# Kernel optimization log

Hardware: AMD Instinct MI355X
Metric: run time of the kernel (lower is better)

The kernel has to match this reference:

```python
import jax, jax.numpy as jnp
import numpy as np

H = 7      # n_hazards
B = 8      # batch
S = 2048   # seq_len
D = 768    # hidden_dim
K = 64     # bottleneck_dim
THR = 0.05 # influence_threshold


def setup_inputs() -> dict:
    key = jax.random.key(0)
    k0, k1, k2, k3 = jax.random.split(key, 4)
    x = jax.random.normal(k0, (H, B, S, D), jnp.float32)          # stacked hazard reprs
    M = jax.random.normal(k1, (H, H), jnp.float32) * 0.3           # interaction_matrix [src, tgt]
    W1 = jax.random.normal(k2, (H, H, D, K), jnp.float32) * (1.0 / np.sqrt(D).astype(np.float32))
    b1 = jnp.zeros((H, H, K), jnp.float32)
    W2 = jax.random.normal(k3, (H, H, K, D), jnp.float32) * (1.0 / np.sqrt(K).astype(np.float32))
    b2 = jnp.zeros((H, H, D), jnp.float32)
    return {"x": x, "M": M, "W1": W1, "b1": b1, "W2": W2, "b2": b2}


def reference(x, M, W1, b1, W2, b2):
    # Gate: influence used only if |M[s,t]| > threshold and s != t (torch skips the
    # projection entirely below threshold; masking to 0 yields identical values/grads).
    eye = jnp.eye(H, dtype=bool)
    gate = jnp.where((jnp.abs(M) > THR) & (~eye), M, jnp.zeros_like(M))  # [s, t]

    # Bottleneck MLP for all (source, target) pairs in one batched GEMM.
    # h: [s, t, b, n, k]
    h = jnp.einsum('sbnd,stdk->stbnk', x, W1) + b1[:, :, None, None, :]
    h = jax.nn.gelu(h, approximate=False)  # torch nn.GELU default is exact (erf)

    # Fold the scalar gate into the second GEMM so the [s,t,b,n,D] tensor is never
    # materialized; sum over sources lands directly at each target.
    add = jnp.einsum('st,stbnk,stkd->tbnd', gate, h, W2)
    add = add + jnp.einsum('st,std->td', gate, b2)[:, None, None, :]
    return x + add  # [H, B, S, D] stacked in hazard order
```

## Files before the change

### kernel.cpp

```cpp
#include <hip/hip_runtime.h>
#include <hip/hip_bf16.h>
#include <math.h>

#define NH   7
#define NROW 16384
#define DD   768
#define KK   64
#define THRG 0.05f

typedef float  f32x4   __attribute__((ext_vector_type(4)));
typedef __bf16 bf16x8  __attribute__((ext_vector_type(8)));
typedef short  short8v __attribute__((ext_vector_type(8)));
typedef short  short4v __attribute__((ext_vector_type(4)));

union V8 { short8v s; bf16x8 b; };

__device__ __forceinline__ unsigned short f2bf(float f) {
  unsigned u = __float_as_uint(f);
  u = (u + 0x7FFFu + ((u >> 16) & 1u)) >> 16;
  return (unsigned short)u;
}

__device__ __forceinline__ float gate_of(const float* __restrict__ M, int s, int t) {
  float m = M[s * NH + t];
  return (s != t && fabsf(m) > THRG) ? m : 0.0f;
}

__device__ __forceinline__ float gelu_t(float v) {
  float u = 0.7978845608028654f * (v + 0.044715f * v * v * v);
  return v / (1.0f + __expf(-2.0f * u));
}

__global__ void prep_w1(const float* __restrict__ W1, unsigned short* __restrict__ W1P) {
  int pr = blockIdx.x;
  const float* src = W1 + (size_t)pr * DD * KK;
  unsigned short* dst = W1P + (size_t)pr * 12 * 4096;
  for (int idx = threadIdx.x; idx < 12 * 64 * 64; idx += blockDim.x) {
    int kc = idx >> 12, rem = idx & 4095;
    int kcol = rem >> 6, dl = rem & 63;
    dst[idx] = f2bf(src[(size_t)(kc * 64 + dl) * KK + kcol]);
  }
}

__global__ void prep_w2(const float* __restrict__ M, const float* __restrict__ W2,
                        unsigned short* __restrict__ W2P) {
  int st = blockIdx.x;
  int s = st / NH, t = st % NH;
  float g = gate_of(M, s, t);
  const float* src = W2 + (size_t)st * KK * DD;
  unsigned short* dst = W2P + (size_t)((t * NH + s) * 6) * 8192;
  for (int idx = threadIdx.x; idx < 6 * 128 * 64; idx += blockDim.x) {
    int nb = idx >> 13, rem = idx & 8191;
    int dloc = rem >> 6, k = rem & 63;
    dst[idx] = f2bf(g * src[(size_t)k * DD + nb * 128 + dloc]);
  }
}

__global__ void prep_b2(const float* __restrict__ M, const float* __restrict__ b2,
                        float* __restrict__ b2sum) {
  int idx = blockIdx.x * blockDim.x + threadIdx.x;
  if (idx >= NH * DD) return;
  int t = idx / DD, d = idx % DD;
  float acc = 0.f;
  for (int s = 0; s < NH; ++s)
    acc += gate_of(M, s, t) * b2[(size_t)(s * NH + t) * DD + d];
  b2sum[idx] = acc;
}

__global__ __launch_bounds__(256, 3)
void chiA(const float* __restrict__ x, const float* __restrict__ M,
          const unsigned short* __restrict__ W1P, const float* __restrict__ b1,
          unsigned short* __restrict__ H) {
  __shared__ __align__(16) unsigned short xs[128 * 64];
  __shared__ __align__(16) unsigned short w1s[64 * 64];

  int bid = (int)blockIdx.x;
  int nid = (bid & 7) * 784 + (bid >> 3);
  int rb = nid / 49, pr = nid % 49;
  int s = pr / NH, t = pr % NH;
  if (gate_of(M, s, t) == 0.0f) return;
  int row0 = rb * 128;

  int tid = (int)threadIdx.x;
  int wid = tid >> 6, lane = tid & 63, l16 = lane & 15, l4 = lane >> 4;

  const f32x4 zero = {0.f, 0.f, 0.f, 0.f};
  f32x4 acc[4][2];
#pragma unroll
  for (int m = 0; m < 4; ++m)
#pragma unroll
    for (int n = 0; n < 2; ++n) acc[m][n] = zero;

  const float* xb = x + ((size_t)s * NROW + row0) * DD;
  const unsigned short* w1b = W1P + (size_t)pr * 12 * 4096;

  for (int kc = 0; kc < 12; ++kc) {
    __syncthreads();
#pragma unroll
    for (int r = 0; r < 4; ++r) {
      int L = r * 4096 + tid * 16;
      int row = L >> 7, colB = L & 127;
      const float* gp = xb + (size_t)row * DD + kc * 64 + (colB >> 1);
      f32x4 v0 = *(const f32x4*)gp;
      f32x4 v1 = *(const f32x4*)(gp + 4);
      short8v sv;
      sv[0] = (short)f2bf(v0[0]); sv[1] = (short)f2bf(v0[1]);
      sv[2] = (short)f2bf(v0[2]); sv[3] = (short)f2bf(v0[3]);
      sv[4] = (short)f2bf(v1[0]); sv[5] = (short)f2bf(v1[1]);
      sv[6] = (short)f2bf(v1[2]); sv[7] = (short)f2bf(v1[3]);
      *(short8v*)((char*)xs + (L ^ ((row & 7) << 4))) = sv;
    }
#pragma unroll
    for (int r = 0; r < 2; ++r) {
      int L = r * 4096 + tid * 16;
      int row = L >> 7;
      short8v v = *(const short8v*)((const char*)w1b + (size_t)kc * 8192 + L);
      *(short8v*)((char*)w1s + (L ^ ((row & 7) << 4))) = v;
    }
    __syncthreads();

    V8 af[4][2], bf2[2][2];
#pragma unroll
    for (int mm = 0; mm < 4; ++mm)
#pragma unroll
      for (int k2 = 0; k2 < 2; ++k2) {
        int rowl = mm * 16 + l16;
        int byte = (rowl * 128 + k2 * 64 + l4 * 16) ^ ((rowl & 7) << 4);
        af[mm][k2].s = *(const short8v*)((const char*)w1s + byte);
      }
#pragma unroll
    for (int nn = 0; nn < 2; ++nn)
#pragma unroll
      for (int k2 = 0; k2 < 2; ++k2) {
        int xr = wid * 32 + nn * 16 + l16;
        int byte = (xr * 128 + k2 * 64 + l4 * 16) ^ ((xr & 7) << 4);
        bf2[nn][k2].s = *(const short8v*)((const char*)xs + byte);
      }
#pragma unroll
    for (int k2 = 0; k2 < 2; ++k2)
#pragma unroll
      for (int mm = 0; mm < 4; ++mm)
#pragma unroll
        for (int nn = 0; nn < 2; ++nn)
          acc[mm][nn] = __builtin_amdgcn_mfma_f32_16x16x32_bf16(af[mm][k2].b, bf2[nn][k2].b, acc[mm][nn], 0, 0, 0);
  }

#pragma unroll
  for (int mm = 0; mm < 4; ++mm) {
    f32x4 bv = *(const f32x4*)(b1 + (size_t)pr * KK + mm * 16 + l4 * 4);
#pragma unroll
    for (int nn = 0; nn < 2; ++nn) {
      short4v o;
#pragma unroll
      for (int r = 0; r < 4; ++r) o[r] = (short)f2bf(gelu_t(acc[mm][nn][r] + bv[r]));
      int xrow = row0 + wid * 32 + nn * 16 + l16;
      unsigned short* hp = H + ((size_t)pr * NROW + xrow) * KK + mm * 16 + l4 * 4;
      *(short4v*)hp = o;
    }
  }
}

__global__ __launch_bounds__(256, 3)
void chiB(const unsigned short* __restrict__ H, const float* __restrict__ x,
          const float* __restrict__ M, const unsigned short* __restrict__ W2P,
          const float* __restrict__ b2sum, float* __restrict__ out) {
  __shared__ __align__(16) unsigned short hs[128 * 64];
  __shared__ __align__(16) unsigned short w2s[128 * 64];

  int bid = (int)blockIdx.x;
  int nid = (bid & 7) * 672 + (bid >> 3);
  int nb = nid % 6, rem = nid / 6;
  int rb = rem % 128, t = rem / 128;
  int row0 = rb * 128, col0 = nb * 128;

  int tid = (int)threadIdx.x;
  int wid = tid >> 6, lane = tid & 63, l16 = lane & 15, l4 = lane >> 4;
  int wm = wid >> 1, wn = wid & 1;

  const f32x4 zero = {0.f, 0.f, 0.f, 0.f};
  f32x4 acc[4][4];
#pragma unroll
  for (int m = 0; m < 4; ++m)
#pragma unroll
    for (int n = 0; n < 4; ++n) acc[m][n] = zero;

  for (int s = 0; s < NH; ++s) {
    if (gate_of(M, s, t) == 0.0f) continue;
    __syncthreads();
    const char* hb = (const char*)(H + ((size_t)(s * NH + t) * NROW + row0) * KK);
    const char* wb = (const char*)(W2P + (size_t)((t * NH + s) * 6 + nb) * 8192);
#pragma unroll
    for (int r = 0; r < 4; ++r) {
      int L = r * 4096 + tid * 16;
      int row = L >> 7;
      short8v v = *(const short8v*)(hb + L);
      *(short8v*)((char*)hs + (L ^ ((row & 7) << 4))) = v;
      short8v w = *(const short8v*)(wb + L);
      *(short8v*)((char*)w2s + (L ^ ((row & 7) << 4))) = w;
    }
    __syncthreads();

    V8 af[4][2], bf2[4][2];
#pragma unroll
    for (int m = 0; m < 4; ++m)
#pragma unroll
      for (int k2 = 0; k2 < 2; ++k2) {
        int rowl = wm * 64 + m * 16 + l16;
        int byte = (rowl * 128 + k2 * 64 + l4 * 16) ^ ((rowl & 7) << 4);
        af[m][k2].s = *(const short8v*)((const char*)hs + byte);
      }
#pragma unroll
    for (int n = 0; n < 4; ++n)
#pragma unroll
      for (int k2 = 0; k2 < 2; ++k2) {
        int dl = wn * 64 + n * 16 + l16;
        int byte = (dl * 128 + k2 * 64 + l4 * 16) ^ ((dl & 7) << 4);
        bf2[n][k2].s = *(const short8v*)((const char*)w2s + byte);
      }
#pragma unroll
    for (int k2 = 0; k2 < 2; ++k2)
#pragma unroll
      for (int m = 0; m < 4; ++m)
#pragma unroll
        for (int n = 0; n < 4; ++n)
          acc[m][n] = __builtin_amdgcn_mfma_f32_16x16x32_bf16(af[m][k2].b, bf2[n][k2].b, acc[m][n], 0, 0, 0);
  }

#pragma unroll
  for (int n = 0; n < 4; ++n) {
    int col = col0 + wn * 64 + n * 16 + l16;
    float b2v = b2sum[(size_t)t * DD + col];
#pragma unroll
    for (int m = 0; m < 4; ++m) {
#pragma unroll
      for (int r = 0; r < 4; ++r) {
        int row = row0 + wm * 64 + m * 16 + l4 * 4 + r;
        size_t off = ((size_t)t * NROW + row) * DD + col;
        out[off] = acc[m][n][r] + x[off] + b2v;
      }
    }
  }
}

extern "C" void kernel_launch(void* const* d_in, const int* in_sizes, int n_in,
                              void* d_out, int out_size, void* d_ws, size_t ws_size,
                              hipStream_t stream) {
  const float* x  = (const float*)d_in[0];
  const float* M  = (const float*)d_in[1];
  const float* W1 = (const float*)d_in[2];
  const float* b1 = (const float*)d_in[3];
  const float* W2 = (const float*)d_in[4];
  const float* b2 = (const float*)d_in[5];
  float* out = (float*)d_out;

  char* ws = (char*)d_ws;
  unsigned short* W1P = (unsigned short*)ws;
  unsigned short* W2P = (unsigned short*)(ws + 4816896);
  float* b2sum        = (float*)(ws + 9633792);
  unsigned short* H   = (unsigned short*)(ws + 9655296);

  prep_w1<<<dim3(49), dim3(256), 0, stream>>>(W1, W1P);
  prep_w2<<<dim3(49), dim3(256), 0, stream>>>(M, W2, W2P);
  prep_b2<<<dim3((NH * DD + 255) / 256), dim3(256), 0, stream>>>(M, b2, b2sum);
  chiA<<<dim3(128 * 49), dim3(256), 0, stream>>>(x, M, W1P, b1, H);
  chiB<<<dim3(NH * 128 * 6), dim3(256), 0, stream>>>(H, x, M, W2P, b2sum, out);
}
```

Before: 488.7 us.

## Fuse both bottleneck GEMMs into one kernel keeping hidden activations in LDS

Replaces the two-kernel pipeline (first GEMM writes bf16 hidden activations to global memory, second GEMM reads them back) with one fused kernel per (target, 128-row block). That kernel computes the hidden tile for every active source into shared memory, then runs the second GEMM from LDS with W2 read straight from global. The first stage is double-buffered, with async global-to-LDS loads for W1 and register-staged x conversion. This removes the global round trip of H and the extra launch, but raises LDS use to 144KB per block. It also cuts the grid to 896 blocks of 512 threads, which may limit occupancy.

```diff
diff --git a/kernel.cpp b/kernel.cpp
--- a/kernel.cpp
+++ b/kernel.cpp
@@ -1,5 +1,4 @@
 #include <hip/hip_runtime.h>
-#include <hip/hip_bf16.h>
 #include <math.h>
 
 #define NH   7
@@ -31,14 +30,21 @@
   return v / (1.0f + __expf(-2.0f * u));
 }
 
+__device__ __forceinline__ void gload_lds16(const void* g, void* l) {
+  __builtin_amdgcn_global_load_lds(
+      (const __attribute__((address_space(1))) unsigned int*)g,
+      (__attribute__((address_space(3))) unsigned int*)l, 16, 0, 0);
+}
+
 __global__ void prep_w1(const float* __restrict__ W1, unsigned short* __restrict__ W1P) {
   int pr = blockIdx.x;
   const float* src = W1 + (size_t)pr * DD * KK;
   unsigned short* dst = W1P + (size_t)pr * 12 * 4096;
-  for (int idx = threadIdx.x; idx < 12 * 64 * 64; idx += blockDim.x) {
+  for (int idx = threadIdx.x; idx < 12 * 4096; idx += blockDim.x) {
     int kc = idx >> 12, rem = idx & 4095;
     int kcol = rem >> 6, dl = rem & 63;
-    dst[idx] = f2bf(src[(size_t)(kc * 64 + dl) * KK + kcol]);
+    int dl_log = dl ^ ((kcol & 7) << 3);
+    dst[idx] = f2bf(src[(size_t)(kc * 64 + dl_log) * KK + kcol]);
   }
 }
 
@@ -48,11 +54,10 @@
   int s = st / NH, t = st % NH;
   float g = gate_of(M, s, t);
   const float* src = W2 + (size_t)st * KK * DD;
-  unsigned short* dst = W2P + (size_t)((t * NH + s) * 6) * 8192;
-  for (int idx = threadIdx.x; idx < 6 * 128 * 64; idx += blockDim.x) {
-    int nb = idx >> 13, rem = idx & 8191;
-    int dloc = rem >> 6, k = rem & 63;
-    dst[idx] = f2bf(g * src[(size_t)k * DD + nb * 128 + dloc]);
+  unsigned short* dst = W2P + (size_t)(t * NH + s) * DD * KK;
+  for (int idx = threadIdx.x; idx < DD * KK; idx += blockDim.x) {
+    int d = idx >> 6, k = idx & 63;
+    dst[idx] = f2bf(g * src[(size_t)k * DD + d]);
   }
 }
 
@@ -67,176 +72,179 @@
   b2sum[idx] = acc;
 }
 
-__global__ __launch_bounds__(256, 3)
-void chiA(const float* __restrict__ x, const float* __restrict__ M,
+__global__ __launch_bounds__(512, 2)
+void chiF(const float* __restrict__ x, const float* __restrict__ M,
           const unsigned short* __restrict__ W1P, const float* __restrict__ b1,
-          unsigned short* __restrict__ H) {
-  __shared__ __align__(16) unsigned short xs[128 * 64];
-  __shared__ __align__(16) unsigned short w1s[64 * 64];
+          const unsigned short* __restrict__ W2P, const float* __restrict__ b2sum,
+          float* __restrict__ out) {
+  extern __shared__ char smem[];
+  unsigned short* Hs = (unsigned short*)smem;
+  char* xsb = smem + 98304;
+  char* w1b = smem + 131072;
 
   int bid = (int)blockIdx.x;
-  int nid = (bid & 7) * 784 + (bid >> 3);
-  int rb = nid / 49, pr = nid % 49;
-  int s = pr / NH, t = pr % NH;
-  if (gate_of(M, s, t) == 0.0f) return;
+  int nid = (bid & 7) * 112 + (bid >> 3);
+  int t = nid % NH, rb = nid / NH;
   int row0 = rb * 128;
 
   int tid = (int)threadIdx.x;
   int wid = tid >> 6, lane = tid & 63, l16 = lane & 15, l4 = lane >> 4;
 
+  unsigned spack = 0; int nact = 0;
+  for (int s = 0; s < NH; ++s) {
+    if (s == t) continue;
+    if (fabsf(M[s * NH + t]) > THRG) { spack |= (unsigned)s << (3 * nact); ++nact; }
+  }
+
   const f32x4 zero = {0.f, 0.f, 0.f, 0.f};
-  f32x4 acc[4][2];
-#pragma unroll
-  for (int m = 0; m < 4; ++m)
-#pragma unroll
-    for (int n = 0; n < 2; ++n) acc[m][n] = zero;
-
-  const float* xb = x + ((size_t)s * NROW + row0) * DD;
-  const unsigned short* w1b = W1P + (size_t)pr * 12 * 4096;
-
-  for (int kc = 0; kc < 12; ++kc) {
+
+  int mh = wid >> 2, qr = wid & 3;
+  int srow = tid >> 2, ssub = tid & 3;
+
+  f32x4 accA[2][2];
+#pragma unroll
+  for (int mm = 0; mm < 2; ++mm)
+#pragma unroll
+    for (int nn = 0; nn < 2; ++nn) accA[mm][nn] = zero;
+
+  f32x4 xr0, xr1, xr2, xr3;
+
+  auto STAGE = [&](int s, int kc, int p) {
+    const char* wsrc = (const char*)(W1P + ((size_t)(s * NH + t) * 12 + kc) * 4096);
+    gload_lds16(wsrc + tid * 16, w1b + p * 8192 + (wid << 10));
+    const float* gp = x + ((size_t)s * NROW + row0 + srow) * DD + kc * 64 + ssub * 16;
+    xr0 = *(const f32x4*)gp;       xr1 = *(const f32x4*)(gp + 4);
+    xr2 = *(const f32x4*)(gp + 8); xr3 = *(const f32x4*)(gp + 12);
+  };
+
+  auto WRITE = [&](int p) {
+    bf16x8 lo, hi;
+    lo[0] = (__bf16)xr0[0]; lo[1] = (__bf16)xr0[1]; lo[2] = (__bf16)xr0[2]; lo[3] = (__bf16)xr0[3];
+    lo[4] = (__bf16)xr1[0]; lo[5] = (__bf16)xr1[1]; lo[6] = (__bf16)xr1[2]; lo[7] = (__bf16)xr1[3];
+    hi[0] = (__bf16)xr2[0]; hi[1] = (__bf16)xr2[1]; hi[2] = (__bf16)xr2[2]; hi[3] = (__bf16)xr2[3];
+    hi[4] = (__bf16)xr3[0]; hi[5] = (__bf16)xr3[1]; hi[6] = (__bf16)xr3[2]; hi[7] = (__bf16)xr3[3];
+    char* base = xsb + p * 16384;
+    int b0 = srow * 128 + ssub * 32, sw = (srow & 7) << 4;
+    *(bf16x8*)(base + (b0 ^ sw)) = lo;
+    *(bf16x8*)(base + ((b0 + 16) ^ sw)) = hi;
+  };
+
+  auto COMPUTE = [&](int p) {
+    const char* xc = xsb + p * 16384;
+    const char* wc = w1b + p * 8192;
+    V8 af[2][2], bfr[2][2];
+#pragma unroll
+    for (int mm = 0; mm < 2; ++mm)
+#pragma unroll
+      for (int k2 = 0; k2 < 2; ++k2) {
+        int rl = mh * 32 + mm * 16 + l16;
+        af[mm][k2].s = *(const short8v*)(wc + ((rl * 128 + k2 * 64 + l4 * 16) ^ ((rl & 7) << 4)));
+      }
+#pragma unroll
+    for (int nn = 0; nn < 2; ++nn)
+#pragma unroll
+      for (int k2 = 0; k2 < 2; ++k2) {
+        int xrow = qr * 32 + nn * 16 + l16;
+        bfr[nn][k2].s = *(const short8v*)(xc + ((xrow * 128 + k2 * 64 + l4 * 16) ^ ((xrow & 7) << 4)));
+      }
+#pragma unroll
+    for (int k2 = 0; k2 < 2; ++k2)
+#pragma unroll
+      for (int mm = 0; mm < 2; ++mm)
+#pragma unroll
+        for (int nn = 0; nn < 2; ++nn)
+          accA[mm][nn] = __builtin_amdgcn_mfma_f32_16x16x32_bf16(af[mm][k2].b, bfr[nn][k2].b,
+                                                                 accA[mm][nn], 0, 0, 0);
+  };
+
+  auto EPIA = [&](int s, int slot) {
+    int pr = s * NH + t;
+    char* hb = (char*)(Hs + slot * 8192);
+#pragma unroll
+    for (int mm = 0; mm < 2; ++mm) {
+      f32x4 bv = *(const f32x4*)(b1 + (size_t)pr * KK + mh * 32 + mm * 16 + l4 * 4);
+#pragma unroll
+      for (int nn = 0; nn < 2; ++nn) {
+        union { short4v s4; __bf16 b4[4]; } o;
+#pragma unroll
+        for (int r = 0; r < 4; ++r) o.b4[r] = (__bf16)gelu_t(accA[mm][nn][r] + bv[r]);
+        int xrow = qr * 32 + nn * 16 + l16;
+        *(short4v*)(hb + ((xrow * 128 + mh * 64 + mm * 32 + l4 * 8) ^ ((xrow & 7) << 4))) = o.s4;
+        accA[mm][nn] = zero;
+      }
+    }
+  };
+
+  if (nact > 0) {
+    const int NSTEP = nact * 12;
+    STAGE(spack & 7, 0, 0);
+    WRITE(0);
     __syncthreads();
-#pragma unroll
-    for (int r = 0; r < 4; ++r) {
-      int L = r * 4096 + tid * 16;
-      int row = L >> 7, colB = L & 127;
-      const float* gp = xb + (size_t)row * DD + kc * 64 + (colB >> 1);
-      f32x4 v0 = *(const f32x4*)gp;
-      f32x4 v1 = *(const f32x4*)(gp + 4);
-      short8v sv;
-      sv[0] = (short)f2bf(v0[0]); sv[1] = (short)f2bf(v0[1]);
-      sv[2] = (short)f2bf(v0[2]); sv[3] = (short)f2bf(v0[3]);
-      sv[4] = (short)f2bf(v1[0]); sv[5] = (short)f2bf(v1[1]);
-      sv[6] = (short)f2bf(v1[2]); sv[7] = (short)f2bf(v1[3]);
-      *(short8v*)((char*)xs + (L ^ ((row & 7) << 4))) = sv;
-    }
-#pragma unroll
-    for (int r = 0; r < 2; ++r) {
-      int L = r * 4096 + tid * 16;
-      int row = L >> 7;
-      short8v v = *(const short8v*)((const char*)w1b + (size_t)kc * 8192 + L);
-      *(short8v*)((char*)w1s + (L ^ ((row & 7) << 4))) = v;
-    }
-    __syncthreads();
-
-    V8 af[4][2], bf2[2][2];
-#pragma unroll
-    for (int mm = 0; mm < 4; ++mm)
-#pragma unroll
-      for (int k2 = 0; k2 < 2; ++k2) {
-        int rowl = mm * 16 + l16;
-        int byte = (rowl * 128 + k2 * 64 + l4 * 16) ^ ((rowl & 7) << 4);
-        af[mm][k2].s = *(const short8v*)((const char*)w1s + byte);
-      }
-#pragma unroll
-    for (int nn = 0; nn < 2; ++nn)
-#pragma unroll
-      for (int k2 = 0; k2 < 2; ++k2) {
-        int xr = wid * 32 + nn * 16 + l16;
-        int byte = (xr * 128 + k2 * 64 + l4 * 16) ^ ((xr & 7) << 4);
-        bf2[nn][k2].s = *(const short8v*)((const char*)xs + byte);
-      }
-#pragma unroll
-    for (int k2 = 0; k2 < 2; ++k2)
-#pragma unroll
-      for (int mm = 0; mm < 4; ++mm)
-#pragma unroll
-        for (int nn = 0; nn < 2; ++nn)
-          acc[mm][nn] = __builtin_amdgcn_mfma_f32_16x16x32_bf16(af[mm][k2].b, bf2[nn][k2].b, acc[mm][nn], 0, 0, 0);
-  }
-
-#pragma unroll
-  for (int mm = 0; mm < 4; ++mm) {
-    f32x4 bv = *(const f32x4*)(b1 + (size_t)pr * KK + mm * 16 + l4 * 4);
-#pragma unroll
-    for (int nn = 0; nn < 2; ++nn) {
-      short4v o;
-#pragma unroll
-      for (int r = 0; r < 4; ++r) o[r] = (short)f2bf(gelu_t(acc[mm][nn][r] + bv[r]));
-      int xrow = row0 + wid * 32 + nn * 16 + l16;
-      unsigned short* hp = H + ((size_t)pr * NROW + xrow) * KK + mm * 16 + l4 * 4;
-      *(short4v*)hp = o;
-    }
-  }
-}
-
-__global__ __launch_bounds__(256, 3)
-void chiB(const unsigned short* __restrict__ H, const float* __restrict__ x,
-          const float* __restrict__ M, const unsigned short* __restrict__ W2P,
-          const float* __restrict__ b2sum, float* __restrict__ out) {
-  __shared__ __align__(16) unsigned short hs[128 * 64];
-  __shared__ __align__(16) unsigned short w2s[128 * 64];
-
-  int bid = (int)blockIdx.x;
-  int nid = (bid & 7) * 672 + (bid >> 3);
-  int nb = nid % 6, rem = nid / 6;
-  int rb = rem % 128, t = rem / 128;
-  int row0 = rb * 128, col0 = nb * 128;
-
-  int tid = (int)threadIdx.x;
-  int wid = tid >> 6, lane = tid & 63, l16 = lane & 15, l4 = lane >> 4;
-  int wm = wid >> 1, wn = wid & 1;
-
-  const f32x4 zero = {0.f, 0.f, 0.f, 0.f};
-  f32x4 acc[4][4];
-#pragma unroll
-  for (int m = 0; m < 4; ++m)
-#pragma unroll
-    for (int n = 0; n < 4; ++n) acc[m][n] = zero;
-
-  for (int s = 0; s < NH; ++s) {
-    if (gate_of(M, s, t) == 0.0f) continue;
-    __syncthreads();
-    const char* hb = (const char*)(H + ((size_t)(s * NH + t) * NROW + row0) * KK);
-    const char* wb = (const char*)(W2P + (size_t)((t * NH + s) * 6 + nb) * 8192);
-#pragma unroll
-    for (int r = 0; r < 4; ++r) {
-      int L = r * 4096 + tid * 16;
-      int row = L >> 7;
-      short8v v = *(const short8v*)(hb + L);
-      *(short8v*)((char*)hs + (L ^ ((row & 7) << 4))) = v;
-      short8v w = *(const short8v*)(wb + L);
-      *(short8v*)((char*)w2s + (L ^ ((row & 7) << 4))) = w;
-    }
-    __syncthreads();
-
-    V8 af[4][2], bf2[4][2];
+    int si = 0, kc = 0;
+    for (int step = 0; step < NSTEP; ++step) {
+      int p = step & 1;
+      int kn = kc + 1, sn = si;
+      if (kn == 12) { kn = 0; sn = si + 1; }
+      bool more = (step + 1 < NSTEP);
+      if (more) STAGE((spack >> (3 * sn)) & 7, kn, p ^ 1);
+      COMPUTE(p);
+      if (more) WRITE(p ^ 1);
+      if (kc == 11) EPIA((spack >> (3 * si)) & 7, si);
+      __syncthreads();
+      kc = kn; si = sn;
+    }
+  }
+
+  int wr = wid & 1, wc = wid >> 1;
+#pragma unroll 1
+  for (int cb = 0; cb < 3; ++cb) {
+    int colb = cb * 256 + wc * 64;
+    f32x4 acc[4][4];
 #pragma unroll
     for (int m = 0; m < 4; ++m)
 #pragma unroll
-      for (int k2 = 0; k2 < 2; ++k2) {
-        int rowl = wm * 64 + m * 16 + l16;
-        int byte = (rowl * 128 + k2 * 64 + l4 * 16) ^ ((rowl & 7) << 4);
-        af[m][k2].s = *(const short8v*)((const char*)hs + byte);
-      }
-#pragma unroll
-    for (int n = 0; n < 4; ++n)
-#pragma unroll
-      for (int k2 = 0; k2 < 2; ++k2) {
-        int dl = wn * 64 + n * 16 + l16;
-        int byte = (dl * 128 + k2 * 64 + l4 * 16) ^ ((dl & 7) << 4);
-        bf2[n][k2].s = *(const short8v*)((const char*)w2s + byte);
-      }
-#pragma unroll
-    for (int k2 = 0; k2 < 2; ++k2)
+      for (int n = 0; n < 4; ++n) acc[m][n] = zero;
+
+    for (int i = 0; i < nact; ++i) {
+      int s = (spack >> (3 * i)) & 7;
+      const char* wp = (const char*)(W2P + ((size_t)(t * NH + s) * DD + colb) * KK);
+      const char* hb = (const char*)(Hs + i * 8192);
+      V8 af[4][2], bfr[4][2];
 #pragma unroll
       for (int m = 0; m < 4; ++m)
 #pragma unroll
-        for (int n = 0; n < 4; ++n)
-          acc[m][n] = __builtin_amdgcn_mfma_f32_16x16x32_bf16(af[m][k2].b, bf2[n][k2].b, acc[m][n], 0, 0, 0);
-  }
-
-#pragma unroll
-  for (int n = 0; n < 4; ++n) {
-    int col = col0 + wn * 64 + n * 16 + l16;
-    float b2v = b2sum[(size_t)t * DD + col];
+        for (int k2 = 0; k2 < 2; ++k2)
+          af[m][k2].s = *(const short8v*)(wp + (m * 16 + l16) * 128 + k2 * 64 + l4 * 16);
+#pragma unroll
+      for (int n = 0; n < 4; ++n)
+#pragma unroll
+        for (int k2 = 0; k2 < 2; ++k2) {
+          int xrow = wr * 64 + n * 16 + l16;
+          bfr[n][k2].s = *(const short8v*)(hb + ((xrow * 128 + k2 * 64 + l4 * 16) ^ ((xrow & 7) << 4)));
+        }
+#pragma unroll
+      for (int k2 = 0; k2 < 2; ++k2)
+#pragma unroll
+        for (int m = 0; m < 4; ++m)
+#pragma unroll
+          for (int n = 0; n < 4; ++n)
+            acc[m][n] = __builtin_amdgcn_mfma_f32_16x16x32_bf16(af[m][k2].b, bfr[n][k2].b,
+                                                                acc[m][n], 0, 0, 0);
+    }
+
 #pragma unroll
     for (int m = 0; m < 4; ++m) {
-#pragma unroll
-      for (int r = 0; r < 4; ++r) {
-        int row = row0 + wm * 64 + m * 16 + l4 * 4 + r;
+      int col = colb + m * 16 + l4 * 4;
+      f32x4 bv = *(const f32x4*)(b2sum + (size_t)t * DD + col);
+#pragma unroll
+      for (int n = 0; n < 4; ++n) {
+        int row = row0 + wr * 64 + n * 16 + l16;
         size_t off = ((size_t)t * NROW + row) * DD + col;
-        out[off] = acc[m][n][r] + x[off] + b2v;
+        f32x4 xv = *(const f32x4*)(x + off);
+        f32x4 ov;
+#pragma unroll
+        for (int r = 0; r < 4; ++r) ov[r] = acc[m][n][r] + xv[r] + bv[r];
+        *(f32x4*)(out + off) = ov;
       }
     }
   }
@@ -257,11 +265,16 @@
   unsigned short* W1P = (unsigned short*)ws;
   unsigned short* W2P = (unsigned short*)(ws + 4816896);
   float* b2sum        = (float*)(ws + 9633792);
-  unsigned short* H   = (unsigned short*)(ws + 9655296);
+
+  static bool attr_set = false;
+  if (!attr_set) {
+    (void)hipFuncSetAttribute((const void*)chiF,
+                              hipFuncAttributeMaxDynamicSharedMemorySize, 147456);
+    attr_set = true;
+  }
 
   prep_w1<<<dim3(49), dim3(256), 0, stream>>>(W1, W1P);
   prep_w2<<<dim3(49), dim3(256), 0, stream>>>(M, W2, W2P);
   prep_b2<<<dim3((NH * DD + 255) / 256), dim3(256), 0, stream>>>(M, b2, b2sum);
-  chiA<<<dim3(128 * 49), dim3(256), 0, stream>>>(x, M, W1P, b1, H);
-  chiB<<<dim3(NH * 128 * 6), dim3(256), 0, stream>>>(H, x, M, W2P, b2sum, out);
-}
+  chiF<<<dim3(896), dim3(512), 147456, stream>>>(x, M, W1P, b1, W2P, b2sum, out);
+}
```

Result: slower. 688.1 us (+40.8%).

## Double-buffer LDS with async global_load_lds and vectorize epilogue stores

Applied to the files above, without the earlier changes.

chiA now double-buffers its x and W1 tiles: W1 goes through async global_load_lds with a pre-swizzled layout and x is prefetched into registers while the previous tile computes. chiB double-buffers H tiles through global_load_lds, reads W2 fragments straight from global memory in a new layout, and swaps the GEMM operand roles so the epilogue can issue float4 loads of x and float4 stores to out. H is written in a pre-swizzled blocked layout so it can be copied straight into LDS. This aims to hide load latency and cut strided scalar output traffic, at the cost of more LDS per block and uncached global reads of W2 fragments.

```diff
diff --git a/kernel.cpp b/kernel.cpp
--- a/kernel.cpp
+++ b/kernel.cpp
@@ -1,5 +1,4 @@
 #include <hip/hip_runtime.h>
-#include <hip/hip_bf16.h>
 #include <math.h>
 
 #define NH   7
@@ -31,14 +30,21 @@
   return v / (1.0f + __expf(-2.0f * u));
 }
 
+__device__ __forceinline__ void gload_lds16(const void* g, void* l) {
+  __builtin_amdgcn_global_load_lds(
+      (const __attribute__((address_space(1))) unsigned int*)g,
+      (__attribute__((address_space(3))) unsigned int*)l, 16, 0, 0);
+}
+
 __global__ void prep_w1(const float* __restrict__ W1, unsigned short* __restrict__ W1P) {
   int pr = blockIdx.x;
   const float* src = W1 + (size_t)pr * DD * KK;
   unsigned short* dst = W1P + (size_t)pr * 12 * 4096;
-  for (int idx = threadIdx.x; idx < 12 * 64 * 64; idx += blockDim.x) {
+  for (int idx = threadIdx.x; idx < 12 * 4096; idx += blockDim.x) {
     int kc = idx >> 12, rem = idx & 4095;
     int kcol = rem >> 6, dl = rem & 63;
-    dst[idx] = f2bf(src[(size_t)(kc * 64 + dl) * KK + kcol]);
+    int dl_log = dl ^ ((kcol & 7) << 3);
+    dst[idx] = f2bf(src[(size_t)(kc * 64 + dl_log) * KK + kcol]);
   }
 }
 
@@ -48,11 +54,10 @@
   int s = st / NH, t = st % NH;
   float g = gate_of(M, s, t);
   const float* src = W2 + (size_t)st * KK * DD;
-  unsigned short* dst = W2P + (size_t)((t * NH + s) * 6) * 8192;
-  for (int idx = threadIdx.x; idx < 6 * 128 * 64; idx += blockDim.x) {
-    int nb = idx >> 13, rem = idx & 8191;
-    int dloc = rem >> 6, k = rem & 63;
-    dst[idx] = f2bf(g * src[(size_t)k * DD + nb * 128 + dloc]);
+  unsigned short* dst = W2P + (size_t)(t * NH + s) * DD * KK;
+  for (int idx = threadIdx.x; idx < DD * KK; idx += blockDim.x) {
+    int d = idx >> 6, k = idx & 63;
+    dst[idx] = f2bf(g * src[(size_t)k * DD + d]);
   }
 }
 
@@ -71,8 +76,8 @@
 void chiA(const float* __restrict__ x, const float* __restrict__ M,
           const unsigned short* __restrict__ W1P, const float* __restrict__ b1,
           unsigned short* __restrict__ H) {
-  __shared__ __align__(16) unsigned short xs[128 * 64];
-  __shared__ __align__(16) unsigned short w1s[64 * 64];
+  __shared__ __align__(16) unsigned short xs[2][128 * 64];
+  __shared__ __align__(16) unsigned short w1s[2][64 * 64];
 
   int bid = (int)blockIdx.x;
   int nid = (bid & 7) * 784 + (bid >> 3);
@@ -84,6 +89,9 @@
   int tid = (int)threadIdx.x;
   int wid = tid >> 6, lane = tid & 63, l16 = lane & 15, l4 = lane >> 4;
 
+  const float* xb = x + ((size_t)s * NROW + row0) * DD;
+  const char* w1b = (const char*)(W1P + (size_t)pr * 12 * 4096);
+
   const f32x4 zero = {0.f, 0.f, 0.f, 0.f};
   f32x4 acc[4][2];
 #pragma unroll
@@ -91,71 +99,91 @@
 #pragma unroll
     for (int n = 0; n < 2; ++n) acc[m][n] = zero;
 
-  const float* xb = x + ((size_t)s * NROW + row0) * DD;
-  const unsigned short* w1b = W1P + (size_t)pr * 12 * 4096;
-
+  int xro = tid >> 3;
+  int xco = (tid & 7) * 8;
+  int sw = (xro & 7) << 4;
+
+  f32x4 xr[8];
+
+  auto STAGE = [&](int kc, int p) {
+    const char* wsrc = w1b + (size_t)kc * 8192;
+    char* wdst = (char*)w1s[p] + (wid << 10);
+#pragma unroll
+    for (int r = 0; r < 2; ++r)
+      gload_lds16(wsrc + r * 4096 + tid * 16, wdst + r * 4096);
+#pragma unroll
+    for (int r = 0; r < 4; ++r) {
+      const float* gp = xb + (size_t)(r * 32 + xro) * DD + kc * 64 + xco;
+      xr[2 * r]     = *(const f32x4*)gp;
+      xr[2 * r + 1] = *(const f32x4*)(gp + 4);
+    }
+  };
+
+  auto WRITE = [&](int p) {
+#pragma unroll
+    for (int r = 0; r < 4; ++r) {
+      bf16x8 v;
+      v[0] = (__bf16)xr[2*r][0]; v[1] = (__bf16)xr[2*r][1];
+      v[2] = (__bf16)xr[2*r][2]; v[3] = (__bf16)xr[2*r][3];
+      v[4] = (__bf16)xr[2*r+1][0]; v[5] = (__bf16)xr[2*r+1][1];
+      v[6] = (__bf16)xr[2*r+1][2]; v[7] = (__bf16)xr[2*r+1][3];
+      int L = r * 4096 + tid * 16;
+      *(bf16x8*)((char*)xs[p] + (L ^ sw)) = v;
+    }
+  };
+
+  auto COMPUTE = [&](int p) {
+    V8 af[4][2], bf2[2][2];
+#pragma unroll
+    for (int mm = 0; mm < 4; ++mm)
+#pragma unroll
+      for (int k2 = 0; k2 < 2; ++k2) {
+        int rl = mm * 16 + l16;
+        af[mm][k2].s = *(const short8v*)((const char*)w1s[p] +
+                         ((rl * 128 + k2 * 64 + l4 * 16) ^ ((rl & 7) << 4)));
+      }
+#pragma unroll
+    for (int nn = 0; nn < 2; ++nn)
+#pragma unroll
+      for (int k2 = 0; k2 < 2; ++k2) {
+        int rl = wid * 32 + nn * 16 + l16;
+        bf2[nn][k2].s = *(const short8v*)((const char*)xs[p] +
+                          ((rl * 128 + k2 * 64 + l4 * 16) ^ ((rl & 7) << 4)));
+      }
+#pragma unroll
+    for (int k2 = 0; k2 < 2; ++k2)
+#pragma unroll
+      for (int mm = 0; mm < 4; ++mm)
+#pragma unroll
+        for (int nn = 0; nn < 2; ++nn)
+          acc[mm][nn] = __builtin_amdgcn_mfma_f32_16x16x32_bf16(af[mm][k2].b, bf2[nn][k2].b,
+                                                                acc[mm][nn], 0, 0, 0);
+  };
+
+  STAGE(0, 0);
+  WRITE(0);
+  __syncthreads();
+  int p = 0;
   for (int kc = 0; kc < 12; ++kc) {
+    bool more = (kc + 1 < 12);
+    if (more) STAGE(kc + 1, p ^ 1);
+    COMPUTE(p);
+    if (more) WRITE(p ^ 1);
     __syncthreads();
-#pragma unroll
-    for (int r = 0; r < 4; ++r) {
-      int L = r * 4096 + tid * 16;
-      int row = L >> 7, colB = L & 127;
-      const float* gp = xb + (size_t)row * DD + kc * 64 + (colB >> 1);
-      f32x4 v0 = *(const f32x4*)gp;
-      f32x4 v1 = *(const f32x4*)(gp + 4);
-      short8v sv;
-      sv[0] = (short)f2bf(v0[0]); sv[1] = (short)f2bf(v0[1]);
-      sv[2] = (short)f2bf(v0[2]); sv[3] = (short)f2bf(v0[3]);
-      sv[4] = (short)f2bf(v1[0]); sv[5] = (short)f2bf(v1[1]);
-      sv[6] = (short)f2bf(v1[2]); sv[7] = (short)f2bf(v1[3]);
-      *(short8v*)((char*)xs + (L ^ ((row & 7) << 4))) = sv;
-    }
-#pragma unroll
-    for (int r = 0; r < 2; ++r) {
-      int L = r * 4096 + tid * 16;
-      int row = L >> 7;
-      short8v v = *(const short8v*)((const char*)w1b + (size_t)kc * 8192 + L);
-      *(short8v*)((char*)w1s + (L ^ ((row & 7) << 4))) = v;
-    }
-    __syncthreads();
-
-    V8 af[4][2], bf2[2][2];
-#pragma unroll
-    for (int mm = 0; mm < 4; ++mm)
-#pragma unroll
-      for (int k2 = 0; k2 < 2; ++k2) {
-        int rowl = mm * 16 + l16;
-        int byte = (rowl * 128 + k2 * 64 + l4 * 16) ^ ((rowl & 7) << 4);
-        af[mm][k2].s = *(const short8v*)((const char*)w1s + byte);
-      }
-#pragma unroll
-    for (int nn = 0; nn < 2; ++nn)
-#pragma unroll
-      for (int k2 = 0; k2 < 2; ++k2) {
-        int xr = wid * 32 + nn * 16 + l16;
-        int byte = (xr * 128 + k2 * 64 + l4 * 16) ^ ((xr & 7) << 4);
-        bf2[nn][k2].s = *(const short8v*)((const char*)xs + byte);
-      }
-#pragma unroll
-    for (int k2 = 0; k2 < 2; ++k2)
-#pragma unroll
-      for (int mm = 0; mm < 4; ++mm)
-#pragma unroll
-        for (int nn = 0; nn < 2; ++nn)
-          acc[mm][nn] = __builtin_amdgcn_mfma_f32_16x16x32_bf16(af[mm][k2].b, bf2[nn][k2].b, acc[mm][nn], 0, 0, 0);
-  }
-
+    p ^= 1;
+  }
+
+  unsigned short* Hb = H + ((size_t)pr * 128 + rb) * 8192;
 #pragma unroll
   for (int mm = 0; mm < 4; ++mm) {
     f32x4 bv = *(const f32x4*)(b1 + (size_t)pr * KK + mm * 16 + l4 * 4);
 #pragma unroll
     for (int nn = 0; nn < 2; ++nn) {
-      short4v o;
-#pragma unroll
-      for (int r = 0; r < 4; ++r) o[r] = (short)f2bf(gelu_t(acc[mm][nn][r] + bv[r]));
-      int xrow = row0 + wid * 32 + nn * 16 + l16;
-      unsigned short* hp = H + ((size_t)pr * NROW + xrow) * KK + mm * 16 + l4 * 4;
-      *(short4v*)hp = o;
+      union { short4v s4; __bf16 b4[4]; } o;
+#pragma unroll
+      for (int r = 0; r < 4; ++r) o.b4[r] = (__bf16)gelu_t(acc[mm][nn][r] + bv[r]);
+      int rl = wid * 32 + nn * 16 + l16;
+      *(short4v*)((char*)Hb + ((rl * 128 + mm * 32 + l4 * 8) ^ ((rl & 7) << 4))) = o.s4;
     }
   }
 }
@@ -164,8 +192,7 @@
 void chiB(const unsigned short* __restrict__ H, const float* __restrict__ x,
           const float* __restrict__ M, const unsigned short* __restrict__ W2P,
           const float* __restrict__ b2sum, float* __restrict__ out) {
-  __shared__ __align__(16) unsigned short hs[128 * 64];
-  __shared__ __align__(16) unsigned short w2s[128 * 64];
+  __shared__ __align__(16) unsigned short hs[2][128 * 64];
 
   int bid = (int)blockIdx.x;
   int nid = (bid & 7) * 672 + (bid >> 3);
@@ -175,7 +202,13 @@
 
   int tid = (int)threadIdx.x;
   int wid = tid >> 6, lane = tid & 63, l16 = lane & 15, l4 = lane >> 4;
-  int wm = wid >> 1, wn = wid & 1;
+  int wr = wid & 1, wc = wid >> 1;
+
+  unsigned spack = 0; int nact = 0;
+  for (int s = 0; s < NH; ++s) {
+    if (s == t) continue;
+    if (fabsf(M[s * NH + t]) > THRG) { spack |= (unsigned)s << (3 * nact); ++nact; }
+  }
 
   const f32x4 zero = {0.f, 0.f, 0.f, 0.f};
   f32x4 acc[4][4];
@@ -184,60 +217,61 @@
 #pragma unroll
     for (int n = 0; n < 4; ++n) acc[m][n] = zero;
 
-  for (int s = 0; s < NH; ++s) {
-    if (gate_of(M, s, t) == 0.0f) continue;
-    __syncthreads();
-    const char* hb = (const char*)(H + ((size_t)(s * NH + t) * NROW + row0) * KK);
-    const char* wb = (const char*)(W2P + (size_t)((t * NH + s) * 6 + nb) * 8192);
-#pragma unroll
-    for (int r = 0; r < 4; ++r) {
-      int L = r * 4096 + tid * 16;
-      int row = L >> 7;
-      short8v v = *(const short8v*)(hb + L);
-      *(short8v*)((char*)hs + (L ^ ((row & 7) << 4))) = v;
-      short8v w = *(const short8v*)(wb + L);
-      *(short8v*)((char*)w2s + (L ^ ((row & 7) << 4))) = w;
-    }
-    __syncthreads();
-
-    V8 af[4][2], bf2[4][2];
-#pragma unroll
-    for (int m = 0; m < 4; ++m)
-#pragma unroll
-      for (int k2 = 0; k2 < 2; ++k2) {
-        int rowl = wm * 64 + m * 16 + l16;
-        int byte = (rowl * 128 + k2 * 64 + l4 * 16) ^ ((rowl & 7) << 4);
-        af[m][k2].s = *(const short8v*)((const char*)hs + byte);
-      }
-#pragma unroll
-    for (int n = 0; n < 4; ++n)
-#pragma unroll
-      for (int k2 = 0; k2 < 2; ++k2) {
-        int dl = wn * 64 + n * 16 + l16;
-        int byte = (dl * 128 + k2 * 64 + l4 * 16) ^ ((dl & 7) << 4);
-        bf2[n][k2].s = *(const short8v*)((const char*)w2s + byte);
-      }
-#pragma unroll
-    for (int k2 = 0; k2 < 2; ++k2)
+  auto GLOADH = [&](int s, int p) {
+    const char* src = (const char*)H + ((size_t)(s * NH + t) * 128 + rb) * 16384;
+    char* dst = (char*)hs[p] + (wid << 10);
+#pragma unroll
+    for (int r = 0; r < 4; ++r)
+      gload_lds16(src + r * 4096 + tid * 16, dst + r * 4096);
+  };
+
+  if (nact > 0) {
+    GLOADH(spack & 7, 0);
+    int p = 0;
+    for (int i = 0; i < nact; ++i) {
+      __syncthreads();
+      if (i + 1 < nact) GLOADH((spack >> (3 * (i + 1))) & 7, p ^ 1);
+      int s = (spack >> (3 * i)) & 7;
+      const char* wp = (const char*)(W2P + ((size_t)(t * NH + s) * DD + col0 + wc * 64) * KK);
+      V8 af[4][2], bfr[4][2];
 #pragma unroll
       for (int m = 0; m < 4; ++m)
 #pragma unroll
-        for (int n = 0; n < 4; ++n)
-          acc[m][n] = __builtin_amdgcn_mfma_f32_16x16x32_bf16(af[m][k2].b, bf2[n][k2].b, acc[m][n], 0, 0, 0);
-  }
-
-#pragma unroll
-  for (int n = 0; n < 4; ++n) {
-    int col = col0 + wn * 64 + n * 16 + l16;
-    float b2v = b2sum[(size_t)t * DD + col];
-#pragma unroll
-    for (int m = 0; m < 4; ++m) {
-#pragma unroll
-      for (int r = 0; r < 4; ++r) {
-        int row = row0 + wm * 64 + m * 16 + l4 * 4 + r;
-        size_t off = ((size_t)t * NROW + row) * DD + col;
-        out[off] = acc[m][n][r] + x[off] + b2v;
-      }
+        for (int k2 = 0; k2 < 2; ++k2)
+          af[m][k2].s = *(const short8v*)(wp + (((m * 16 + l16) * 64 + k2 * 32 + l4 * 8) * 2));
+#pragma unroll
+      for (int n = 0; n < 4; ++n)
+#pragma unroll
+        for (int k2 = 0; k2 < 2; ++k2) {
+          int rl = wr * 64 + n * 16 + l16;
+          bfr[n][k2].s = *(const short8v*)((const char*)hs[p] +
+                           ((rl * 128 + k2 * 64 + l4 * 16) ^ ((rl & 7) << 4)));
+        }
+#pragma unroll
+      for (int k2 = 0; k2 < 2; ++k2)
+#pragma unroll
+        for (int m = 0; m < 4; ++m)
+#pragma unroll
+          for (int n = 0; n < 4; ++n)
+            acc[m][n] = __builtin_amdgcn_mfma_f32_16x16x32_bf16(af[m][k2].b, bfr[n][k2].b,
+                                                                acc[m][n], 0, 0, 0);
+      p ^= 1;
+    }
+  }
+
+#pragma unroll
+  for (int m = 0; m < 4; ++m) {
+    int col = col0 + wc * 64 + m * 16 + l4 * 4;
+    f32x4 bv = *(const f32x4*)(b2sum + (size_t)t * DD + col);
+#pragma unroll
+    for (int n = 0; n < 4; ++n) {
+      int row = row0 + wr * 64 + n * 16 + l16;
+      size_t off = ((size_t)t * NROW + row) * DD + col;
+      f32x4 xv = *(const f32x4*)(x + off);
+      f32x4 ov;
+#pragma unroll
+      for (int r = 0; r < 4; ++r) ov[r] = acc[m][n][r] + xv[r] + bv[r];
+      *(f32x4*)(out + off) = ov;
     }
   }
 }
```

After: 574.6 us. 1.18x slower.
